# Kernel optimization log

Hardware: AMD Instinct MI355X
Metric: run time of the kernel (lower is better)

Reference implementation:

```python
import jax, jax.numpy as jnp
import numpy as np

NUM_EXPERTS = 8
HIDDEN = 1024
INTER = 1024
BATCH = 2
SEQ = 1024
TOP_K = 2
SWIGLU_ALPHA = 1.702
LIMIT = 7.0


def setup_inputs() -> dict:
    key = jax.random.key(0)
    ks = jax.random.split(key, 7)
    hidden_states = jax.random.normal(ks[0], (BATCH, SEQ, HIDDEN), jnp.float32)
    router_indices = jax.random.randint(ks[1], (BATCH * SEQ, TOP_K), 0, NUM_EXPERTS)
    routing_weights = jax.nn.softmax(
        jax.random.normal(ks[2], (BATCH * SEQ, NUM_EXPERTS), jnp.float32), axis=-1)
    scale = 0.02
    gate_up_proj = jax.random.normal(ks[3], (NUM_EXPERTS, HIDDEN, 2 * INTER), jnp.float32) * scale
    gate_up_proj_bias = jax.random.normal(ks[4], (NUM_EXPERTS, 2 * INTER), jnp.float32) * scale
    down_proj = jax.random.normal(ks[5], (NUM_EXPERTS, INTER, HIDDEN), jnp.float32) * scale
    down_proj_bias = jax.random.normal(ks[6], (NUM_EXPERTS, HIDDEN), jnp.float32) * scale
    return {
        "hidden_states": hidden_states,
        "router_indices": router_indices,
        "routing_weights": routing_weights,
        "gate_up_proj": gate_up_proj,
        "gate_up_proj_bias": gate_up_proj_bias,
        "down_proj": down_proj,
        "down_proj_bias": down_proj_bias,
    }


def _grouped_mm(x, w, expert_ids):
    """Grouped GEMM: y[t] = x[t] @ w[expert_ids[t]].

    x: [T, K], w: [E, K, N], expert_ids: [T] int.
    Reference form via one-hot masking (exact equivalent of torch._grouped_mm
    on expert-sorted tokens); guaranteed jit- and grad-safe.
    """
    onehot = jax.nn.one_hot(expert_ids, w.shape[0], dtype=x.dtype)  # [T, E]
    y_all = jnp.einsum('tk,ekn->etn', x, w)                         # [E, T, N]
    return jnp.einsum('te,etn->tn', onehot, y_all)                  # [T, N]


def _gpt_oss_swiglu(x):
    gate = jnp.minimum(x[..., ::2], LIMIT)
    up = jnp.clip(x[..., 1::2], -LIMIT, LIMIT)
    glu = gate * jax.nn.sigmoid(gate * SWIGLU_ALPHA)
    return (up + 1.0) * glu


def reference(hidden_states, router_indices, routing_weights,
              gate_up_proj, gate_up_proj_bias, down_proj, down_proj_bias):
    B = hidden_states.shape[0]
    H = hidden_states.shape[-1]
    x = hidden_states.reshape(-1, H)                       # [M, H]
    M = x.shape[0]
    top_k = router_indices.shape[1]
    num_experts = gate_up_proj.shape[0]

    # routing_weights is [M, num_experts] -> gather the top-k weights
    topk_weights = jnp.take_along_axis(routing_weights, router_indices, axis=1)  # [M, K]

    flat_experts = router_indices.reshape(-1)              # [T = M*K]
    sort_idx = jnp.argsort(flat_experts)                   # expert-sorted order
    sorted_pos = sort_idx // top_k                         # token id per slot
    expert_sorted = flat_experts[sort_idx]                 # [T]
    grouped = x[sorted_pos]                                # [T, H]

    gate_up = _grouped_mm(grouped, gate_up_proj, expert_sorted)
    gate_up = gate_up + gate_up_proj_bias[expert_sorted]   # per-expert bias
    inter = _gpt_oss_swiglu(gate_up)                       # [T, I]

    down = _grouped_mm(inter, down_proj, expert_sorted)
    down = down + down_proj_bias[expert_sorted]            # [T, H]
    down = down * topk_weights.reshape(-1)[sort_idx][:, None]

    out = jnp.zeros((M, H), x.dtype).at[sorted_pos].add(down)  # scatter-add combine
    return out.reshape(B, -1, H)
```

## Files before the change

kernel.cpp:

```cpp
#include <hip/hip_runtime.h>

#define NE 8
#define NH 1024
#define NI 1024
#define NGU 2048
#define MTOK 2048
#define TSLOT 4096

#define MAXT64 80
#define MAXT128 40

typedef short s16x8 __attribute__((ext_vector_type(8)));
typedef float f32x4 __attribute__((ext_vector_type(4)));
typedef unsigned short u16;

#define WS_SEG      0
#define WS_DESC64   64
#define WS_DESC128  384
#define WS_SLOT     1024
#define WS_INTER    32768
#define INTER_ROWS  4224
#define WS_WTGU     8683520UL
#define WS_R        42237952UL
#define WS_NEED_FAST 59015168UL

__device__ inline u16 f2bf(float f) {
    unsigned u = __builtin_bit_cast(unsigned, f);
    u += 0x7fffu + ((u >> 16) & 1u);
    return (u16)(u >> 16);
}

__device__ inline void lds_dma16(const u16* g, u16* l) {
    __builtin_amdgcn_global_load_lds(
        (const __attribute__((address_space(1))) unsigned int*)g,
        (__attribute__((address_space(3))) unsigned int*)l, 16, 0, 0);
}

__device__ inline int lds_off(int row, int blk) {
    return (row << 7) | (((blk ^ (row & 7)) & 7) << 4);
}

__global__ void k_build(const int* __restrict__ ridx, int* __restrict__ seg,
                        int* __restrict__ d64, int* __restrict__ d128,
                        int* __restrict__ slot_of) {
    __shared__ int cnt[NE];
    __shared__ int cur[NE];
    int tid = threadIdx.x;
    if (tid < NE) cnt[tid] = 0;
    __syncthreads();
    for (int s = tid; s < TSLOT; s += blockDim.x) atomicAdd(&cnt[ridx[s] & 7], 1);
    __syncthreads();
    if (tid == 0) {
        int a = 0;
        for (int e = 0; e < NE; ++e) { seg[e] = a; cur[e] = a; a += cnt[e]; }
        seg[NE] = a;
        int nt = 0;
        for (int e = 0; e < NE; ++e)
            for (int m0 = 0; m0 < cnt[e]; m0 += 64) d64[nt++] = (e << 16) | (m0 / 64);
        for (; nt < MAXT64; ++nt) d64[nt] = -1;
        nt = 0;
        for (int e = 0; e < NE; ++e)
            for (int m0 = 0; m0 < cnt[e]; m0 += 128) d128[nt++] = (e << 16) | (m0 / 128);
        for (; nt < MAXT128; ++nt) d128[nt] = -1;
    }
    __syncthreads();
    for (int s = tid; s < TSLOT; s += blockDim.x) {
        int e = ridx[s] & 7;
        int p = atomicAdd(&cur[e], 1);
        slot_of[p] = s;
    }
}

__global__ __launch_bounds__(256) void k_gather(const float* __restrict__ x,
                                                const int* __restrict__ slot_of,
                                                u16* __restrict__ A) {
    int r = blockIdx.x;
    int token = slot_of[r] >> 1;
    float4 v = ((const float4*)(x + (size_t)token * NH))[threadIdx.x];
    ushort4 o;
    o.x = f2bf(v.x); o.y = f2bf(v.y); o.z = f2bf(v.z); o.w = f2bf(v.w);
    ((ushort4*)(A + (size_t)r * NH))[threadIdx.x] = o;
}

__global__ __launch_bounds__(256) void k_tr(const float* __restrict__ W,
                                            u16* __restrict__ WT, int K, int N) {
    __shared__ u16 T[64][72];
    int tid = threadIdx.x;
    const float* in = W + (size_t)blockIdx.z * K * N;
    u16* out = WT + (size_t)blockIdx.z * N * K;
    int n0 = blockIdx.x * 64, k0 = blockIdx.y * 64;
#pragma unroll
    for (int p = 0; p < 4; ++p) {
        int idx = p * 256 + tid;
        int kr = idx >> 4, nc = (idx & 15) * 4;
        float4 v = *(const float4*)(in + (size_t)(k0 + kr) * N + n0 + nc);
        T[nc + 0][kr] = f2bf(v.x); T[nc + 1][kr] = f2bf(v.y);
        T[nc + 2][kr] = f2bf(v.z); T[nc + 3][kr] = f2bf(v.w);
    }
    __syncthreads();
#pragma unroll
    for (int p = 0; p < 2; ++p) {
        int idx = p * 256 + tid;
        int nr = idx >> 3, kc = (idx & 7) * 8;
        s16x8 vv = *(const s16x8*)&T[nr][kc];
        *(s16x8*)(out + (size_t)(n0 + nr) * K + k0 + kc) = vv;
    }
}

__global__ __launch_bounds__(256) void k_gateup_f(
        const u16* __restrict__ A,
        const u16* __restrict__ wt,
        const float* __restrict__ bias,
        const int* __restrict__ seg, const int* __restrict__ desc,
        u16* __restrict__ inter) {
    int d = desc[blockIdx.x];
    if (d < 0) return;
    int e = d >> 16, mt = d & 0xffff;
    int seg0 = seg[e], Te = seg[e + 1] - seg0, m0 = mt * 128;

    __shared__ __align__(16) u16 As[128 * 64];
    __shared__ __align__(16) u16 Bs[64 * 64];

    int tid = threadIdx.x;
    int lane = tid & 63, w = tid >> 6;
    int ml = lane & 15, kq = lane >> 4;
    int wm = w >> 1, wn = w & 1;
    int n0 = blockIdx.y * 64;
    const u16* wte = wt + (size_t)e * NGU * NH;
    int dr = lane >> 3, db = (lane & 7) ^ dr;
    const u16* Ag = A + (size_t)(seg0 + m0) * NH;

    f32x4 zero = {0.f, 0.f, 0.f, 0.f};
    f32x4 acc[4][2];
#pragma unroll
    for (int i = 0; i < 4; ++i) { acc[i][0] = zero; acc[i][1] = zero; }

    for (int kb = 0; kb < NH; kb += 64) {
        __syncthreads();
#pragma unroll
        for (int c = 0; c < 4; ++c) {
            int row = c * 32 + w * 8 + dr;
            lds_dma16(Ag + (size_t)row * NH + kb + db * 8, As + c * 2048 + w * 512);
        }
#pragma unroll
        for (int c = 0; c < 2; ++c) {
            int row = c * 32 + w * 8 + dr;
            lds_dma16(wte + (size_t)(n0 + row) * NH + kb + db * 8, Bs + c * 2048 + w * 512);
        }
        __syncthreads();

#pragma unroll
        for (int kk = 0; kk < 64; kk += 32) {
            s16x8 af[4], bf[2];
#pragma unroll
            for (int i = 0; i < 4; ++i)
                af[i] = *(const s16x8*)((char*)As + lds_off(wm * 64 + i * 16 + ml, (kk >> 3) + kq));
#pragma unroll
            for (int i = 0; i < 2; ++i)
                bf[i] = *(const s16x8*)((char*)Bs + lds_off(wn * 32 + i * 16 + ml, (kk >> 3) + kq));
#pragma unroll
            for (int mi = 0; mi < 4; ++mi)
#pragma unroll
                for (int ni = 0; ni < 2; ++ni)
                    acc[mi][ni] = __builtin_amdgcn_mfma_f32_16x16x32_bf16(
                        af[mi], bf[ni], acc[mi][ni], 0, 0, 0);
        }
    }

#pragma unroll
    for (int ni = 0; ni < 2; ++ni) {
        int n = n0 + wn * 32 + ni * 16 + ml;
        float bv = bias[e * NGU + n];
#pragma unroll
        for (int mi = 0; mi < 4; ++mi) {
#pragma unroll
            for (int r = 0; r < 4; ++r) {
                float v = acc[mi][ni][r] + bv;
                float pr = __shfl_xor(v, 1, 64);
                float g = (lane & 1) ? pr : v;
                float u = (lane & 1) ? v : pr;
                g = fminf(g, 7.0f);
                u = fminf(fmaxf(u, -7.0f), 7.0f);
                float glu = g / (1.0f + __expf(-1.702f * g));
                float y = (u + 1.0f) * glu;
                int mloc = wm * 64 + mi * 16 + kq * 4 + r;
                if (!(lane & 1) && (m0 + mloc) < Te)
                    inter[(size_t)(seg0 + m0 + mloc) * NI + (n >> 1)] = f2bf(y);
            }
        }
    }
}

__global__ __launch_bounds__(256) void k_down_f(
        const u16* __restrict__ inter,
        const u16* __restrict__ wt,
        const float* __restrict__ bias,
        const float* __restrict__ rw,
        const int* __restrict__ seg, const int* __restrict__ desc,
        const int* __restrict__ slot_of,
        float* __restrict__ out) {
    int d = desc[blockIdx.x];
    if (d < 0) return;
    int e = d >> 16, mt = d & 0xffff;
    int seg0 = seg[e], Te = seg[e + 1] - seg0, m0 = mt * 128;
    int kz = blockIdx.z;

    __shared__ __align__(16) u16 As[128 * 64];
    __shared__ __align__(16) u16 Bs[64 * 64];

    int tid = threadIdx.x;
    int lane = tid & 63, w = tid >> 6;
    int ml = lane & 15, kq = lane >> 4;
    int wm = w >> 1, wn = w & 1;
    int n0 = blockIdx.y * 64;
    const u16* wte = wt + (size_t)e * NH * NI;
    int dr = lane >> 3, db = (lane & 7) ^ dr;
    const u16* Ig = inter + (size_t)(seg0 + m0) * NI;

    f32x4 zero = {0.f, 0.f, 0.f, 0.f};
    f32x4 acc[4][2];
#pragma unroll
    for (int i = 0; i < 4; ++i) { acc[i][0] = zero; acc[i][1] = zero; }

    int kbeg = kz * (NI / 2), kend = kbeg + NI / 2;
    for (int kb = kbeg; kb < kend; kb += 64) {
        __syncthreads();
#pragma unroll
        for (int c = 0; c < 4; ++c) {
            int row = c * 32 + w * 8 + dr;
            lds_dma16(Ig + (size_t)row * NI + kb + db * 8, As + c * 2048 + w * 512);
        }
#pragma unroll
        for (int c = 0; c < 2; ++c) {
            int row = c * 32 + w * 8 + dr;
            lds_dma16(wte + (size_t)(n0 + row) * NI + kb + db * 8, Bs + c * 2048 + w * 512);
        }
        __syncthreads();

#pragma unroll
        for (int kk = 0; kk < 64; kk += 32) {
            s16x8 af[4], bf[2];
#pragma unroll
            for (int i = 0; i < 4; ++i)
                af[i] = *(const s16x8*)((char*)As + lds_off(wm * 64 + i * 16 + ml, (kk >> 3) + kq));
#pragma unroll
            for (int i = 0; i < 2; ++i)
                bf[i] = *(const s16x8*)((char*)Bs + lds_off(wn * 32 + i * 16 + ml, (kk >> 3) + kq));
#pragma unroll
            for (int mi = 0; mi < 4; ++mi)
#pragma unroll
                for (int ni = 0; ni < 2; ++ni)
                    acc[mi][ni] = __builtin_amdgcn_mfma_f32_16x16x32_bf16(
                        af[mi], bf[ni], acc[mi][ni], 0, 0, 0);
        }
    }

    float bv[2];
#pragma unroll
    for (int ni = 0; ni < 2; ++ni)
        bv[ni] = (kz == 0) ? bias[e * NH + n0 + wn * 32 + ni * 16 + ml] : 0.0f;

#pragma unroll
    for (int mi = 0; mi < 4; ++mi) {
#pragma unroll
        for (int r = 0; r < 4; ++r) {
            int mloc = wm * 64 + mi * 16 + kq * 4 + r;
            if ((m0 + mloc) < Te) {
                int slot = slot_of[seg0 + m0 + mloc];
                int token = slot >> 1;
                float wgt = rw[token * NE + e];
#pragma unroll
                for (int ni = 0; ni < 2; ++ni) {
                    int n = n0 + wn * 32 + ni * 16 + ml;
                    atomicAdd(&out[(size_t)token * NH + n], (acc[mi][ni][r] + bv[ni]) * wgt);
                }
            }
        }
    }
}

__global__ __launch_bounds__(256) void k_gateup_s(
        const float* __restrict__ x, const float* __restrict__ w,
        const float* __restrict__ bias,
        const int* __restrict__ seg, const int* __restrict__ desc,
        const int* __restrict__ slot_of, u16* __restrict__ inter) {
    int d = desc[blockIdx.x];
    if (d < 0) return;
    int e = d >> 16, mt = d & 0xffff;
    int seg0 = seg[e], Te = seg[e + 1] - seg0, m0 = mt * 64;
    __shared__ u16 As[64 * 40];
    __shared__ int tok[64];
    int tid = threadIdx.x;
    if (tid < 64) {
        int m = m0 + tid;
        tok[tid] = (m < Te) ? (slot_of[seg0 + m] >> 1) : -1;
    }
    __syncthreads();
    int lane = tid & 63, wave = tid >> 6;
    int arow = tid >> 2, acol = (tid & 3) * 8;
    int ta = tok[arow];
    int kq = lane >> 4, ml = lane & 15;
    int nb = blockIdx.y * 128 + wave * 32;
    const float* wp = w + (size_t)e * NH * NGU;
    f32x4 zero = {0.f, 0.f, 0.f, 0.f};
    f32x4 acc[4][2];
#pragma unroll
    for (int i = 0; i < 4; ++i) { acc[i][0] = zero; acc[i][1] = zero; }
    for (int kb = 0; kb < NH; kb += 32) {
        float4 a0 = {0, 0, 0, 0}, a1 = {0, 0, 0, 0};
        if (ta >= 0) {
            const float* xp = x + (size_t)ta * NH + kb + acol;
            a0 = *(const float4*)xp; a1 = *(const float4*)(xp + 4);
        }
        s16x8 av;
        av[0] = (short)f2bf(a0.x); av[1] = (short)f2bf(a0.y);
        av[2] = (short)f2bf(a0.z); av[3] = (short)f2bf(a0.w);
        av[4] = (short)f2bf(a1.x); av[5] = (short)f2bf(a1.y);
        av[6] = (short)f2bf(a1.z); av[7] = (short)f2bf(a1.w);
        __syncthreads();
        *(s16x8*)&As[arow * 40 + acol] = av;
        __syncthreads();
        s16x8 afr[4];
#pragma unroll
        for (int msi = 0; msi < 4; ++msi)
            afr[msi] = *(const s16x8*)&As[(msi * 16 + ml) * 40 + kq * 8];
        s16x8 bfr[2];
#pragma unroll
        for (int s = 0; s < 2; ++s) {
            const float* bp = wp + (size_t)(kb + kq * 8) * NGU + nb + s * 16 + ml;
#pragma unroll
            for (int j = 0; j < 8; ++j) bfr[s][j] = (short)f2bf(bp[(size_t)j * NGU]);
        }
#pragma unroll
        for (int msi = 0; msi < 4; ++msi)
#pragma unroll
            for (int s = 0; s < 2; ++s)
                acc[msi][s] = __builtin_amdgcn_mfma_f32_16x16x32_bf16(
                    afr[msi], bfr[s], acc[msi][s], 0, 0, 0);
    }
#pragma unroll
    for (int s = 0; s < 2; ++s) {
        int n = nb + s * 16 + ml;
        float bv = bias[e * NGU + n];
#pragma unroll
        for (int msi = 0; msi < 4; ++msi) {
#pragma unroll
            for (int r = 0; r < 4; ++r) {
                float v = acc[msi][s][r] + bv;
                float pr = __shfl_xor(v, 1, 64);
                float g = (lane & 1) ? pr : v;
                float u = (lane & 1) ? v : pr;
                g = fminf(g, 7.0f);
                u = fminf(fmaxf(u, -7.0f), 7.0f);
                float glu = g / (1.0f + __expf(-1.702f * g));
                float y = (u + 1.0f) * glu;
                int mrow = m0 + msi * 16 + kq * 4 + r;
                if (!(lane & 1) && mrow < Te)
                    inter[(size_t)(seg0 + mrow) * NI + (n >> 1)] = f2bf(y);
            }
        }
    }
}

__global__ __launch_bounds__(256) void k_down_s(
        const u16* __restrict__ inter, const float* __restrict__ w,
        const float* __restrict__ bias, const float* __restrict__ rw,
        const int* __restrict__ seg, const int* __restrict__ desc,
        const int* __restrict__ slot_of, float* __restrict__ out) {
    int d = desc[blockIdx.x];
    if (d < 0) return;
    int e = d >> 16, mt = d & 0xffff;
    int seg0 = seg[e], Te = seg[e + 1] - seg0, m0 = mt * 64;
    __shared__ u16 As[64 * 40];
    int tid = threadIdx.x;
    int lane = tid & 63, wave = tid >> 6;
    int arow = tid >> 2, acol = (tid & 3) * 8;
    bool avalid = (m0 + arow) < Te;
    int kq = lane >> 4, ml = lane & 15;
    int nb = blockIdx.y * 128 + wave * 32;
    const float* wp = w + (size_t)e * NI * NH;
    f32x4 zero = {0.f, 0.f, 0.f, 0.f};
    f32x4 acc[4][2];
#pragma unroll
    for (int i = 0; i < 4; ++i) { acc[i][0] = zero; acc[i][1] = zero; }
    for (int kb = 0; kb < NI; kb += 32) {
        s16x8 av = {0, 0, 0, 0, 0, 0, 0, 0};
        if (avalid) av = *(const s16x8*)(inter + (size_t)(seg0 + m0 + arow) * NI + kb + acol);
        __syncthreads();
        *(s16x8*)&As[arow * 40 + acol] = av;
        __syncthreads();
        s16x8 afr[4];
#pragma unroll
        for (int msi = 0; msi < 4; ++msi)
            afr[msi] = *(const s16x8*)&As[(msi * 16 + ml) * 40 + kq * 8];
        s16x8 bfr[2];
#pragma unroll
        for (int s = 0; s < 2; ++s) {
            const float* bp = wp + (size_t)(kb + kq * 8) * NH + nb + s * 16 + ml;
#pragma unroll
            for (int j = 0; j < 8; ++j) bfr[s][j] = (short)f2bf(bp[(size_t)j * NH]);
        }
#pragma unroll
        for (int msi = 0; msi < 4; ++msi)
#pragma unroll
            for (int s = 0; s < 2; ++s)
                acc[msi][s] = __builtin_amdgcn_mfma_f32_16x16x32_bf16(
                    afr[msi], bfr[s], acc[msi][s], 0, 0, 0);
    }
    float bv[2];
    bv[0] = bias[e * NH + nb + ml];
    bv[1] = bias[e * NH + nb + 16 + ml];
#pragma unroll
    for (int msi = 0; msi < 4; ++msi) {
#pragma unroll
        for (int r = 0; r < 4; ++r) {
            int mrow = m0 + msi * 16 + kq * 4 + r;
            if (mrow < Te) {
                int slot = slot_of[seg0 + mrow];
                int token = slot >> 1;
                float wgt = rw[token * NE + e];
#pragma unroll
                for (int s = 0; s < 2; ++s) {
                    int n = nb + s * 16 + ml;
                    atomicAdd(&out[(size_t)token * NH + n], (acc[msi][s][r] + bv[s]) * wgt);
                }
            }
        }
    }
}

extern "C" void kernel_launch(void* const* d_in, const int* in_sizes, int n_in,
                              void* d_out, int out_size, void* d_ws, size_t ws_size,
                              hipStream_t stream) {
    const float* x   = (const float*)d_in[0];
    const int*   ri  = (const int*)d_in[1];
    const float* rw  = (const float*)d_in[2];
    const float* wgu = (const float*)d_in[3];
    const float* bgu = (const float*)d_in[4];
    const float* wd  = (const float*)d_in[5];
    const float* bd  = (const float*)d_in[6];
    float* out = (float*)d_out;

    char* ws = (char*)d_ws;
    int* seg     = (int*)(ws + WS_SEG);
    int* d64     = (int*)(ws + WS_DESC64);
    int* d128    = (int*)(ws + WS_DESC128);
    int* slot_of = (int*)(ws + WS_SLOT);
    u16* inter   = (u16*)(ws + WS_INTER);

    hipMemsetAsync(out, 0, (size_t)MTOK * NH * sizeof(float), stream);
    hipLaunchKernelGGL(k_build, dim3(1), dim3(256), 0, stream, ri, seg, d64, d128, slot_of);

    if (ws_size >= WS_NEED_FAST) {
        u16* wtgu  = (u16*)(ws + WS_WTGU);
        u16* regR  = (u16*)(ws + WS_R);
        hipLaunchKernelGGL(k_tr, dim3(NGU / 64, NH / 64, NE), dim3(256), 0, stream,
                           wgu, wtgu, NH, NGU);
        hipLaunchKernelGGL(k_gather, dim3(TSLOT), dim3(256), 0, stream, x, slot_of, regR);
        hipLaunchKernelGGL(k_gateup_f, dim3(MAXT128, NGU / 64), dim3(256), 0, stream,
                           regR, wtgu, bgu, seg, d128, inter);
        hipLaunchKernelGGL(k_tr, dim3(NH / 64, NI / 64, NE), dim3(256), 0, stream,
                           wd, regR, NI, NH);
        hipLaunchKernelGGL(k_down_f, dim3(MAXT128, NH / 64, 2), dim3(256), 0, stream,
                           inter, regR, bd, rw, seg, d128, slot_of, out);
    } else {
        hipLaunchKernelGGL(k_gateup_s, dim3(MAXT64, NGU / 128), dim3(256), 0, stream,
                           x, wgu, bgu, seg, d64, slot_of, inter);
        hipLaunchKernelGGL(k_down_s, dim3(MAXT64, NH / 128), dim3(256), 0, stream,
                           inter, wd, bd, rw, seg, d64, slot_of, out);
    }
}
```

Measured before the change: 245.1 us.

## Replace atomic scatter-add combine with split-K partial buffers and gather combine

The down-projection kernel now writes its split-K partial results as plain stores into two per-slot float buffers instead of atomically adding into the output. A new combine kernel gathers each token's two slots through a new position map, applies the routing weights and writes the output once, which also removes the output memset. The weight-transpose kernel is reworked to pack bf16 pairs into 32-bit shared-memory writes with a tighter padding, and the GEMM row loads clamp at the last slot instead of reading past it. Together these remove atomic contention and the memset, at the cost of writing and re-reading about 32 MB of intermediate buffers plus one extra launch.

```diff
diff --git a/kernel.cpp b/kernel.cpp
--- a/kernel.cpp
+++ b/kernel.cpp
@@ -18,11 +18,12 @@
 #define WS_DESC64   64
 #define WS_DESC128  384
 #define WS_SLOT     1024
-#define WS_INTER    32768
-#define INTER_ROWS  4224
-#define WS_WTGU     8683520UL
-#define WS_R        42237952UL
-#define WS_NEED_FAST 59015168UL
+#define WS_POS      17408
+#define WS_INTER    33792
+#define WS_AREG     8422400UL
+#define WS_WREG     25199616UL
+#define WS_DB_OFF   16777216UL
+#define WS_NEED_FAST 58754048UL
 
 __device__ inline u16 f2bf(float f) {
     unsigned u = __builtin_bit_cast(unsigned, f);
@@ -42,7 +43,7 @@
 
 __global__ void k_build(const int* __restrict__ ridx, int* __restrict__ seg,
                         int* __restrict__ d64, int* __restrict__ d128,
-                        int* __restrict__ slot_of) {
+                        int* __restrict__ slot_of, int* __restrict__ pos_of) {
     __shared__ int cnt[NE];
     __shared__ int cur[NE];
     int tid = threadIdx.x;
@@ -68,6 +69,7 @@
         int e = ridx[s] & 7;
         int p = atomicAdd(&cur[e], 1);
         slot_of[p] = s;
+        pos_of[s] = p;
     }
 }
 
@@ -84,26 +86,36 @@
 
 __global__ __launch_bounds__(256) void k_tr(const float* __restrict__ W,
                                             u16* __restrict__ WT, int K, int N) {
-    __shared__ u16 T[64][72];
+    __shared__ u16 T[64][66];
     int tid = threadIdx.x;
     const float* in = W + (size_t)blockIdx.z * K * N;
     u16* out = WT + (size_t)blockIdx.z * N * K;
     int n0 = blockIdx.x * 64, k0 = blockIdx.y * 64;
 #pragma unroll
-    for (int p = 0; p < 4; ++p) {
-        int idx = p * 256 + tid;
-        int kr = idx >> 4, nc = (idx & 15) * 4;
-        float4 v = *(const float4*)(in + (size_t)(k0 + kr) * N + n0 + nc);
-        T[nc + 0][kr] = f2bf(v.x); T[nc + 1][kr] = f2bf(v.y);
-        T[nc + 2][kr] = f2bf(v.z); T[nc + 3][kr] = f2bf(v.w);
+    for (int p = 0; p < 2; ++p) {
+        int kr = p * 32 + (tid >> 4) * 2;
+        int nc = (tid & 15) * 4;
+        const float* r0 = in + (size_t)(k0 + kr) * N + n0 + nc;
+        float4 v0 = *(const float4*)r0;
+        float4 v1 = *(const float4*)(r0 + N);
+#pragma unroll
+        for (int i = 0; i < 4; ++i) {
+            unsigned lo = f2bf(((const float*)&v0)[i]);
+            unsigned hi = f2bf(((const float*)&v1)[i]);
+            *(unsigned*)&T[nc + i][kr] = lo | (hi << 16);
+        }
     }
     __syncthreads();
 #pragma unroll
     for (int p = 0; p < 2; ++p) {
         int idx = p * 256 + tid;
         int nr = idx >> 3, kc = (idx & 7) * 8;
-        s16x8 vv = *(const s16x8*)&T[nr][kc];
-        *(s16x8*)(out + (size_t)(n0 + nr) * K + k0 + kc) = vv;
+        unsigned q0 = *(const unsigned*)&T[nr][kc + 0];
+        unsigned q1 = *(const unsigned*)&T[nr][kc + 2];
+        unsigned q2 = *(const unsigned*)&T[nr][kc + 4];
+        unsigned q3 = *(const unsigned*)&T[nr][kc + 6];
+        uint4 vv = {q0, q1, q2, q3};
+        *(uint4*)(out + (size_t)(n0 + nr) * K + k0 + kc) = vv;
     }
 }
 
@@ -128,7 +140,6 @@
     int n0 = blockIdx.y * 64;
     const u16* wte = wt + (size_t)e * NGU * NH;
     int dr = lane >> 3, db = (lane & 7) ^ dr;
-    const u16* Ag = A + (size_t)(seg0 + m0) * NH;
 
     f32x4 zero = {0.f, 0.f, 0.f, 0.f};
     f32x4 acc[4][2];
@@ -139,8 +150,9 @@
         __syncthreads();
 #pragma unroll
         for (int c = 0; c < 4; ++c) {
-            int row = c * 32 + w * 8 + dr;
-            lds_dma16(Ag + (size_t)row * NH + kb + db * 8, As + c * 2048 + w * 512);
+            int gr = seg0 + m0 + c * 32 + w * 8 + dr;
+            if (gr > TSLOT - 1) gr = TSLOT - 1;
+            lds_dma16(A + (size_t)gr * NH + kb + db * 8, As + c * 2048 + w * 512);
         }
 #pragma unroll
         for (int c = 0; c < 2; ++c) {
@@ -195,10 +207,9 @@
         const u16* __restrict__ inter,
         const u16* __restrict__ wt,
         const float* __restrict__ bias,
-        const float* __restrict__ rw,
         const int* __restrict__ seg, const int* __restrict__ desc,
-        const int* __restrict__ slot_of,
-        float* __restrict__ out) {
+        float* __restrict__ dA,
+        float* __restrict__ dB) {
     int d = desc[blockIdx.x];
     if (d < 0) return;
     int e = d >> 16, mt = d & 0xffff;
@@ -215,20 +226,20 @@
     int n0 = blockIdx.y * 64;
     const u16* wte = wt + (size_t)e * NH * NI;
     int dr = lane >> 3, db = (lane & 7) ^ dr;
-    const u16* Ig = inter + (size_t)(seg0 + m0) * NI;
 
     f32x4 zero = {0.f, 0.f, 0.f, 0.f};
     f32x4 acc[4][2];
 #pragma unroll
     for (int i = 0; i < 4; ++i) { acc[i][0] = zero; acc[i][1] = zero; }
 
-    int kbeg = kz * (NI / 2), kend = kbeg + NI / 2;
-    for (int kb = kbeg; kb < kend; kb += 64) {
+    int kbeg = kz * (NI / 2);
+    for (int kb = kbeg; kb < kbeg + NI / 2; kb += 64) {
         __syncthreads();
 #pragma unroll
         for (int c = 0; c < 4; ++c) {
-            int row = c * 32 + w * 8 + dr;
-            lds_dma16(Ig + (size_t)row * NI + kb + db * 8, As + c * 2048 + w * 512);
+            int gr = seg0 + m0 + c * 32 + w * 8 + dr;
+            if (gr > TSLOT - 1) gr = TSLOT - 1;
+            lds_dma16(inter + (size_t)gr * NI + kb + db * 8, As + c * 2048 + w * 512);
         }
 #pragma unroll
         for (int c = 0; c < 2; ++c) {
@@ -255,6 +266,7 @@
         }
     }
 
+    float* dst = kz ? dB : dA;
     float bv[2];
 #pragma unroll
     for (int ni = 0; ni < 2; ++ni)
@@ -266,17 +278,38 @@
         for (int r = 0; r < 4; ++r) {
             int mloc = wm * 64 + mi * 16 + kq * 4 + r;
             if ((m0 + mloc) < Te) {
-                int slot = slot_of[seg0 + m0 + mloc];
-                int token = slot >> 1;
-                float wgt = rw[token * NE + e];
+                size_t row = (size_t)(seg0 + m0 + mloc);
 #pragma unroll
                 for (int ni = 0; ni < 2; ++ni) {
                     int n = n0 + wn * 32 + ni * 16 + ml;
-                    atomicAdd(&out[(size_t)token * NH + n], (acc[mi][ni][r] + bv[ni]) * wgt);
+                    dst[row * NH + n] = acc[mi][ni][r] + bv[ni];
                 }
             }
         }
     }
+}
+
+__global__ __launch_bounds__(256) void k_comb(
+        const float* __restrict__ dA, const float* __restrict__ dB,
+        const float* __restrict__ rw, const int* __restrict__ ridx,
+        const int* __restrict__ pos_of, float* __restrict__ out) {
+    int t = blockIdx.x;
+    int h = threadIdx.x * 4;
+    float4 s = {0.f, 0.f, 0.f, 0.f};
+#pragma unroll
+    for (int k = 0; k < 2; ++k) {
+        int slot = t * 2 + k;
+        int e = ridx[slot] & 7;
+        float wgt = rw[t * NE + e];
+        size_t r = (size_t)pos_of[slot];
+        float4 a = *(const float4*)(dA + r * NH + h);
+        float4 b = *(const float4*)(dB + r * NH + h);
+        s.x += wgt * (a.x + b.x);
+        s.y += wgt * (a.y + b.y);
+        s.z += wgt * (a.z + b.z);
+        s.w += wgt * (a.w + b.w);
+    }
+    *(float4*)(out + (size_t)t * NH + h) = s;
 }
 
 __global__ __launch_bounds__(256) void k_gateup_s(
@@ -446,24 +479,31 @@
     int* d64     = (int*)(ws + WS_DESC64);
     int* d128    = (int*)(ws + WS_DESC128);
     int* slot_of = (int*)(ws + WS_SLOT);
+    int* pos_of  = (int*)(ws + WS_POS);
     u16* inter   = (u16*)(ws + WS_INTER);
 
-    hipMemsetAsync(out, 0, (size_t)MTOK * NH * sizeof(float), stream);
-    hipLaunchKernelGGL(k_build, dim3(1), dim3(256), 0, stream, ri, seg, d64, d128, slot_of);
+    hipLaunchKernelGGL(k_build, dim3(1), dim3(256), 0, stream, ri, seg, d64, d128,
+                       slot_of, pos_of);
 
     if (ws_size >= WS_NEED_FAST) {
-        u16* wtgu  = (u16*)(ws + WS_WTGU);
-        u16* regR  = (u16*)(ws + WS_R);
+        u16*   aReg = (u16*)(ws + WS_AREG);
+        float* dA   = (float*)(ws + WS_AREG);
+        u16*   wReg = (u16*)(ws + WS_WREG);
+        float* dB   = (float*)(ws + WS_WREG + WS_DB_OFF);
+
         hipLaunchKernelGGL(k_tr, dim3(NGU / 64, NH / 64, NE), dim3(256), 0, stream,
-                           wgu, wtgu, NH, NGU);
-        hipLaunchKernelGGL(k_gather, dim3(TSLOT), dim3(256), 0, stream, x, slot_of, regR);
+                           wgu, wReg, NH, NGU);
+        hipLaunchKernelGGL(k_gather, dim3(TSLOT), dim3(256), 0, stream, x, slot_of, aReg);
         hipLaunchKernelGGL(k_gateup_f, dim3(MAXT128, NGU / 64), dim3(256), 0, stream,
-                           regR, wtgu, bgu, seg, d128, inter);
+                           aReg, wReg, bgu, seg, d128, inter);
         hipLaunchKernelGGL(k_tr, dim3(NH / 64, NI / 64, NE), dim3(256), 0, stream,
-                           wd, regR, NI, NH);
+                           wd, wReg, NI, NH);
         hipLaunchKernelGGL(k_down_f, dim3(MAXT128, NH / 64, 2), dim3(256), 0, stream,
-                           inter, regR, bd, rw, seg, d128, slot_of, out);
+                           inter, wReg, bd, seg, d128, dA, dB);
+        hipLaunchKernelGGL(k_comb, dim3(MTOK), dim3(256), 0, stream,
+                           dA, dB, rw, ri, pos_of, out);
     } else {
+        hipMemsetAsync(out, 0, (size_t)MTOK * NH * sizeof(float), stream);
         hipLaunchKernelGGL(k_gateup_s, dim3(MAXT64, NGU / 128), dim3(256), 0, stream,
                            x, wgu, bgu, seg, d64, slot_of, inter);
         hipLaunchKernelGGL(k_down_s, dim3(MAXT64, NH / 128), dim3(256), 0, stream,
```

Result: faster. 238.9 us (-2.6%).
